# Performance work log

Hardware: AMD Instinct MI355X
Metric: run time of the kernel (lower is better)

Reference implementation:

```python
import jax, jax.numpy as jnp
import numpy as np
import math

NUM_CLASSES = 91
FOCAL_ALPHA = 0.25
FOCAL_GAMMA = 2.0
BBOX_COEF = 5.0
GIOU_COEF = 2.0
ANGLE_COEF = 1.0
PI = math.pi


def _rect_corners(box):
    # box: [5] = (cx, cy, w, h, theta) -> [4,2] corners, CCW order
    cx, cy, w, h, th = box[0], box[1], box[2], box[3], box[4]
    c, s = jnp.cos(th), jnp.sin(th)
    dx = jnp.array([0.5, -0.5, -0.5, 0.5], box.dtype) * w
    dy = jnp.array([0.5, 0.5, -0.5, -0.5], box.dtype) * h
    px = cx + c * dx - s * dy
    py = cy + s * dx + c * dy
    return jnp.stack([px, py], axis=-1)


def _pair_obb_iou(b1, b2):
    # Oriented-box IoU of one pair via Sutherland-Hodgman convex clipping.
    # Intersection of two convex quads has at most 8 vertices.
    P = _rect_corners(b1)  # subject polygon [4,2]
    Q = _rect_corners(b2)  # clip polygon   [4,2]
    verts = jnp.concatenate([P, jnp.tile(P[:1], (4, 1))], axis=0)  # [8,2] padded
    n = jnp.int32(4)
    cQ = Q.mean(0)
    idx = jnp.arange(8)
    for k in range(4):  # clip against each edge of Q
        a, b = Q[k], Q[(k + 1) % 4]
        ex, ey = b[0] - a[0], b[1] - a[1]
        sd = lambda p: ex * (p[..., 1] - a[1]) - ey * (p[..., 0] - a[0])
        sgn = jnp.where(sd(cQ) >= 0, 1.0, -1.0)
        d = sd(verts) * sgn  # signed distance, >=0 means inside [8]
        nidx = jnp.where(idx == n - 1, 0, idx + 1)
        d_cur, d_nxt = d, d[nidx]
        valid_edge = idx < n
        cur_in, nxt_in = d_cur >= 0, d_nxt >= 0
        denom = d_cur - d_nxt
        t = jnp.where(jnp.abs(denom) > 1e-12, d_cur / jnp.where(denom == 0, 1.0, denom), 0.0)
        inter_pt = verts + t[:, None] * (verts[nidx] - verts)
        out_pts = jnp.zeros((16, 2), verts.dtype)
        out_pts = out_pts.at[0::2].set(inter_pt)
        out_pts = out_pts.at[1::2].set(verts[nidx])
        out_valid = jnp.zeros(16, bool)
        out_valid = out_valid.at[0::2].set(valid_edge & (cur_in != nxt_in))
        out_valid = out_valid.at[1::2].set(valid_edge & nxt_in)
        order = jnp.argsort(~out_valid)  # stable: valid points first, order kept
        verts = out_pts[order][:8]
        n = jnp.minimum(jnp.sum(out_valid), 8).astype(jnp.int32)
    # shoelace area; pad invalid slots with v0 so extra edges contribute 0
    verts = jnp.where((idx < n)[:, None], verts, verts[0][None])
    x, y = verts[:, 0], verts[:, 1]
    inter = 0.5 * jnp.abs(jnp.sum(x * jnp.roll(y, -1) - jnp.roll(x, -1) * y))
    a1 = b1[2] * b1[3]
    a2 = b2[2] * b2[3]
    union = a1 + a2 - inter
    return jnp.where(union > 0, inter / union, 0.0)


def _losses(pred_logits, pred_boxes, tgt_boxes, batch_idx, src_idx, tgt_labels, nb):
    B, Q, C = pred_logits.shape
    # ---- loss_labels: scatter one-hot + sigmoid focal loss ----
    target_classes = jnp.full((B, Q), NUM_CLASSES, jnp.int32)
    target_classes = target_classes.at[batch_idx, src_idx].set(tgt_labels.astype(jnp.int32))
    onehot = jax.nn.one_hot(target_classes, C + 1, dtype=pred_logits.dtype)[..., :C]
    prob = jax.nn.sigmoid(pred_logits)
    ce = jnp.maximum(pred_logits, 0) - pred_logits * onehot + jnp.log1p(jnp.exp(-jnp.abs(pred_logits)))
    p_t = prob * onehot + (1 - prob) * (1 - onehot)
    alpha_t = FOCAL_ALPHA * onehot + (1 - FOCAL_ALPHA) * (1 - onehot)
    focal = alpha_t * ce * (1 - p_t) ** FOCAL_GAMMA
    loss_ce = focal.mean(1).sum() / nb * Q
    # ---- loss_boxes: L1 + angle + oriented IoU ----
    src_boxes = pred_boxes[batch_idx, src_idx]  # [N,5]
    loss_bbox = jnp.abs(src_boxes[:, :4] - tgt_boxes[:, :4]).sum() / nb * BBOX_COEF
    ap, at = src_boxes[:, 4], tgt_boxes[:, 4]
    loss_angle = jnp.minimum(jnp.abs(ap - at), jnp.abs(ap - (at + PI))).sum() / nb * ANGLE_COEF
    iou = jax.vmap(_pair_obb_iou)(src_boxes, tgt_boxes)  # diag of obb_iou(src, tgt)
    loss_giou = (1.0 - iou).sum() / nb * GIOU_COEF
    return jnp.stack([loss_ce, loss_bbox, loss_giou, loss_angle])


def setup_inputs() -> dict:
    key = jax.random.key(0)
    ks = jax.random.split(key, 8)
    B, Q, C, N = 128, 900, 91, 8192
    pred_logits = jax.random.normal(ks[0], (B, Q, C), jnp.float32)
    def make_boxes(k, shape):
        k1, k2, k3 = jax.random.split(k, 3)
        xy = jax.random.uniform(k1, shape[:-1] + (2,), jnp.float32)
        wh = jax.random.uniform(k2, shape[:-1] + (2,), jnp.float32) * 0.2 + 0.05
        th = jax.random.uniform(k3, shape[:-1] + (1,), jnp.float32) * PI
        return jnp.concatenate([xy, wh, th], axis=-1)
    pred_boxes = make_boxes(ks[1], (B, Q, 5))
    tgt_boxes = make_boxes(ks[2], (N, 5))
    batch_idx = jnp.sort(jax.random.randint(ks[3], (N,), 0, B))
    src_idx = jax.random.randint(ks[4], (N,), 0, Q)
    tgt_labels = jax.random.randint(ks[5], (N,), 0, C)
    return {"pred_logits": pred_logits, "pred_boxes": pred_boxes, "tgt_boxes": tgt_boxes,
            "batch_idx": batch_idx, "src_idx": src_idx, "tgt_labels": tgt_labels, "num_boxes": N}


def reference(pred_logits, pred_boxes, tgt_boxes, batch_idx, src_idx, tgt_labels, num_boxes):
    nb = jnp.asarray(num_boxes, jnp.float32)
    return _losses(pred_logits, pred_boxes, tgt_boxes, batch_idx, src_idx, tgt_labels, nb)
```

## Files before the change

kernel.cpp:

```cpp
#include <hip/hip_runtime.h>
#include <math.h>

#define QN 900
#define CN 91
#define NPAIR 8192
#define PI_F 3.14159265358979323846f

#define PAIR_BLOCKS 32
#define FOCAL_BLOCKS 2048
#define NFLOAT4 (128 * 900 * CN / 4)


__device__ __forceinline__ float read_nb(const void* p) {
    int iv = *(const int*)p;
    if (iv > 0 && iv < (1 << 30)) return (float)iv;
    return *(const float*)p;
}

__device__ __forceinline__ float f0_raw(float x) {
    float e   = __expf(-fabsf(x));
    float ope = 1.0f + e;
    float r   = __builtin_amdgcn_rcpf(ope);
    float l   = __logf(ope);
    float sp  = fmaxf(x, 0.0f) + l;
    float s   = (x >= 0.0f) ? r : e * r;
    return sp * s * s;
}


__device__ void focal_body(int rb, const float4* __restrict__ l4, const void* nbp,
                           float* out, float* sm) {
    float acc = 0.0f;
    const int stride = FOCAL_BLOCKS * 256;
    for (int i = rb * 256 + threadIdx.x; i < NFLOAT4; i += stride) {
        float4 v = l4[i];
        acc += f0_raw(v.x);
        acc += f0_raw(v.y);
        acc += f0_raw(v.z);
        acc += f0_raw(v.w);
    }
#pragma unroll
    for (int o = 32; o > 0; o >>= 1) acc += __shfl_down(acc, o, 64);
    int lane = threadIdx.x & 63, w = threadIdx.x >> 6;
    if (lane == 0) sm[w] = acc;
    __syncthreads();
    if (threadIdx.x == 0) {
        float nb = read_nb(nbp);
        atomicAdd(out + 0, (sm[0] + sm[1] + sm[2] + sm[3]) * 0.75f / nb);
    }
}

__device__ void pairs_body(const float* __restrict__ logits,
                           const float* __restrict__ pb, const float* __restrict__ tb,
                           const int* __restrict__ bi, const int* __restrict__ si,
                           const int* __restrict__ lbl,
                           const void* nbp, float* out, float* sm) {
    int i = blockIdx.x * 256 + threadIdx.x;
    int b = bi[i], s = si[i], label = lbl[i];
    int slot = b * QN + s;

    bool is_last = true;
    for (int j = i + 1; j < NPAIR; ++j) {
        if (bi[j] != b) break;
        if (si[j] == s) { is_last = false; break; }
    }

    float corr = 0.0f;
    if (is_last) {
        float x = logits[slot * CN + label];
        float e   = __expf(-fabsf(x));
        float ope = 1.0f + e;
        float r   = __builtin_amdgcn_rcpf(ope);
        float l   = __logf(ope);
        float sp_p = fmaxf(x, 0.0f) + l;
        float sp_n = fmaxf(-x, 0.0f) + l;
        float sg  = (x >= 0.0f) ? r : e * r;
        float oms = 1.0f - sg;
        corr = 0.25f * sp_n * oms * oms - 0.75f * sp_p * sg * sg;
    }

    const float* p = pb + slot * 5;
    const float* t = tb + i * 5;
    float p0 = p[0], p1 = p[1], p2 = p[2], p3 = p[3], p4 = p[4];
    float t0 = t[0], t1 = t[1], t2 = t[2], t3 = t[3], t4 = t[4];

    float lb = fabsf(p0 - t0) + fabsf(p1 - t1) + fabsf(p2 - t2) + fabsf(p3 - t3);
    float la = fminf(fabsf(p4 - t4), fabsf(p4 - (t4 + PI_F)));

    const float dxs[4] = {0.5f, -0.5f, -0.5f, 0.5f};
    const float dys[4] = {0.5f, 0.5f, -0.5f, -0.5f};
    float c1 = cosf(p4), s1 = sinf(p4);
    float c2 = cosf(t4), s2 = sinf(t4);
    float px[8], py[8], qx[4], qy[4];
#pragma unroll
    for (int k = 0; k < 4; k++) {
        float dx = dxs[k] * p2, dy = dys[k] * p3;
        px[k] = p0 + c1 * dx - s1 * dy;
        py[k] = p1 + s1 * dx + c1 * dy;
        float ex = dxs[k] * t2, ey = dys[k] * t3;
        qx[k] = t0 + c2 * ex - s2 * ey;
        qy[k] = t1 + s2 * ex + c2 * ey;
    }
#pragma unroll
    for (int k = 4; k < 8; k++) { px[k] = 0.0f; py[k] = 0.0f; }
    float cqx = (qx[0] + qx[1] + qx[2] + qx[3]) * 0.25f;
    float cqy = (qy[0] + qy[1] + qy[2] + qy[3]) * 0.25f;

    int n = 4;
#pragma unroll
    for (int k = 0; k < 4; k++) {
        float ax = qx[k], ay = qy[k];
        int k2 = (k + 1) & 3;
        float ex = qx[k2] - ax, ey = qy[k2] - ay;
        float sd_c = ex * (cqy - ay) - ey * (cqx - ax);
        float sgn = (sd_c >= 0.0f) ? 1.0f : -1.0f;
        float d[8];
#pragma unroll
        for (int ii = 0; ii < 8; ii++)
            d[ii] = sgn * (ex * (py[ii] - ay) - ey * (px[ii] - ax));
        float nx[8], ny[8];
#pragma unroll
        for (int ii = 0; ii < 8; ii++) { nx[ii] = 0.0f; ny[ii] = 0.0f; }
        int m = 0;
#pragma unroll
        for (int ii = 0; ii < 8; ii++) {
            bool act  = ii < n;
            bool last = (ii == n - 1);
            float jx = last ? px[0] : (ii < 7 ? px[ii + 1] : 0.0f);
            float jy = last ? py[0] : (ii < 7 ? py[ii + 1] : 0.0f);
            float dn = last ? d[0]  : (ii < 7 ? d[ii + 1]  : 0.0f);
            float dc = d[ii];
            bool ci = dc >= 0.0f, ni_ = dn >= 0.0f;
            bool emitI = act && (ci != ni_);
            bool emitV = act && ni_;
            float den = dc - dn;
            float tt = (fabsf(den) > 1e-12f) ? (dc / den) : 0.0f;
            float ix = px[ii] + tt * (jx - px[ii]);
            float iy = py[ii] + tt * (jy - py[ii]);
#pragma unroll
            for (int ss = 0; ss < 8; ss++) {
                bool w1 = emitI && (ss == m);
                nx[ss] = w1 ? ix : nx[ss];
                ny[ss] = w1 ? iy : ny[ss];
            }
            m += emitI ? 1 : 0;
#pragma unroll
            for (int ss = 0; ss < 8; ss++) {
                bool w2 = emitV && (ss == m);
                nx[ss] = w2 ? jx : nx[ss];
                ny[ss] = w2 ? jy : ny[ss];
            }
            m += emitV ? 1 : 0;
        }
#pragma unroll
        for (int ii = 0; ii < 8; ii++) { px[ii] = nx[ii]; py[ii] = ny[ii]; }
        n = (m > 8) ? 8 : m;
    }
    float a2 = 0.0f;
#pragma unroll
    for (int ii = 0; ii < 8; ii++) {
        bool act  = ii < n;
        bool last = (ii == n - 1);
        float jx = last ? px[0] : (ii < 7 ? px[ii + 1] : 0.0f);
        float jy = last ? py[0] : (ii < 7 ? py[ii + 1] : 0.0f);
        a2 += act ? (px[ii] * jy - jx * py[ii]) : 0.0f;
    }
    float inter = 0.5f * fabsf(a2);
    float uni = p2 * p3 + t2 * t3 - inter;
    float iou = (uni > 0.0f) ? inter / uni : 0.0f;
    float lg = 1.0f - iou;

#pragma unroll
    for (int o = 32; o > 0; o >>= 1) {
        lb   += __shfl_down(lb, o, 64);
        lg   += __shfl_down(lg, o, 64);
        la   += __shfl_down(la, o, 64);
        corr += __shfl_down(corr, o, 64);
    }
    int lane = threadIdx.x & 63, w = threadIdx.x >> 6;
    if (lane == 0) { sm[w] = lb; sm[4 + w] = lg; sm[8 + w] = la; sm[12 + w] = corr; }
    __syncthreads();
    if (threadIdx.x == 0) {
        float nb = read_nb(nbp);
        float inv = 1.0f / nb;
        atomicAdd(out + 0, (sm[12] + sm[13] + sm[14] + sm[15]) * inv);
        atomicAdd(out + 1, (sm[0] + sm[1] + sm[2] + sm[3]) * 5.0f * inv);
        atomicAdd(out + 2, (sm[4] + sm[5] + sm[6] + sm[7]) * 2.0f * inv);
        atomicAdd(out + 3, (sm[8] + sm[9] + sm[10] + sm[11]) * inv);
    }
}


__global__ __launch_bounds__(256) void mega_kernel(const float* __restrict__ logits,
                                                   const float* __restrict__ pboxes,
                                                   const float* __restrict__ tboxes,
                                                   const int* __restrict__ bidx,
                                                   const int* __restrict__ sidx,
                                                   const int* __restrict__ labels,
                                                   const void* __restrict__ nbp,
                                                   float* __restrict__ out) {
    __shared__ float sm[16];
    int rb = blockIdx.x;
    if (rb < PAIR_BLOCKS) {
        pairs_body(logits, pboxes, tboxes, bidx, sidx, labels, nbp, out, sm);
    } else {
        focal_body(rb - PAIR_BLOCKS, (const float4*)logits, nbp, out, sm);
    }
}


extern "C" void kernel_launch(void* const* d_in, const int* in_sizes, int n_in,
                              void* d_out, int out_size, void* d_ws, size_t ws_size,
                              hipStream_t stream) {
    const float* logits = (const float*)d_in[0];
    const float* pboxes = (const float*)d_in[1];
    const float* tboxes = (const float*)d_in[2];
    const int*   bidx   = (const int*)d_in[3];
    const int*   sidx   = (const int*)d_in[4];
    const int*   labels = (const int*)d_in[5];
    const void*  nbp    = d_in[6];
    float* out = (float*)d_out;

    mega_kernel<<<PAIR_BLOCKS + FOCAL_BLOCKS, 256, 0, stream>>>(
        logits, pboxes, tboxes, bidx, sidx, labels, nbp, out);
}
```

Measured before the change: 130.8 us.

## Replace global atomics with workspace partials plus reduction kernel; stage dedup scan in LDS

Each block now writes its partial sums to a workspace slot, and a second single-block kernel reduces them and applies the num_boxes normalization. This replaces the per-block atomicAdds to the output, which also removes the dependence on the output being zeroed beforehand. The duplicate-slot check in the pair blocks now scans a 384-entry window of batch and src indices staged in shared memory, and falls back to global loads only when the run extends past that window. The cost is one extra kernel launch plus some shared memory per block.

```diff
diff --git a/kernel.cpp b/kernel.cpp
--- a/kernel.cpp
+++ b/kernel.cpp
@@ -8,7 +8,9 @@
 
 #define PAIR_BLOCKS 32
 #define FOCAL_BLOCKS 2048
+#define TOTAL_BLOCKS (PAIR_BLOCKS + FOCAL_BLOCKS)
 #define NFLOAT4 (128 * 900 * CN / 4)
+#define BSCAN 384
 
 
 __device__ __forceinline__ float read_nb(const void* p) {
@@ -28,8 +30,8 @@
 }
 
 
-__device__ void focal_body(int rb, const float4* __restrict__ l4, const void* nbp,
-                           float* out, float* sm) {
+__device__ void focal_body(int rb, const float4* __restrict__ l4,
+                           float4* __restrict__ ws, float* sm) {
     float acc = 0.0f;
     const int stride = FOCAL_BLOCKS * 256;
     for (int i = rb * 256 + threadIdx.x; i < NFLOAT4; i += stride) {
@@ -44,29 +46,42 @@
     int lane = threadIdx.x & 63, w = threadIdx.x >> 6;
     if (lane == 0) sm[w] = acc;
     __syncthreads();
-    if (threadIdx.x == 0) {
-        float nb = read_nb(nbp);
-        atomicAdd(out + 0, (sm[0] + sm[1] + sm[2] + sm[3]) * 0.75f / nb);
-    }
+    if (threadIdx.x == 0)
+        ws[blockIdx.x] = make_float4((sm[0] + sm[1] + sm[2] + sm[3]) * 0.75f,
+                                     0.0f, 0.0f, 0.0f);
 }
 
 __device__ void pairs_body(const float* __restrict__ logits,
                            const float* __restrict__ pb, const float* __restrict__ tb,
                            const int* __restrict__ bi, const int* __restrict__ si,
                            const int* __restrict__ lbl,
-                           const void* nbp, float* out, float* sm) {
-    int i = blockIdx.x * 256 + threadIdx.x;
-    int b = bi[i], s = si[i], label = lbl[i];
+                           float4* __restrict__ ws, float* sm,
+                           int* sb, int* ss) {
+    int base = blockIdx.x * 256;
+    for (int k = threadIdx.x; k < BSCAN; k += 256) {
+        int g = base + k;
+        sb[k] = (g < NPAIR) ? bi[g] : -1;
+        ss[k] = (g < NPAIR) ? si[g] : -1;
+    }
+    __syncthreads();
+
+    int i = base + threadIdx.x;
+    int b = sb[threadIdx.x], s = ss[threadIdx.x], label = lbl[i];
     int slot = b * QN + s;
 
-    bool is_last = true;
-    for (int j = i + 1; j < NPAIR; ++j) {
-        if (bi[j] != b) break;
-        if (si[j] == s) { is_last = false; break; }
+    int bad = 0;
+#pragma unroll 4
+    for (int k = threadIdx.x + 1; k < BSCAN; ++k)
+        bad |= (sb[k] == b) & (ss[k] == s);
+    if (!bad && sb[BSCAN - 1] == b) {
+        for (int j = base + BSCAN; j < NPAIR; ++j) {
+            if (bi[j] != b) break;
+            if (si[j] == s) { bad = 1; break; }
+        }
     }
 
     float corr = 0.0f;
-    if (is_last) {
+    if (!bad) {
         float x = logits[slot * CN + label];
         float e   = __expf(-fabsf(x));
         float ope = 1.0f + e;
@@ -138,17 +153,17 @@
             float ix = px[ii] + tt * (jx - px[ii]);
             float iy = py[ii] + tt * (jy - py[ii]);
 #pragma unroll
-            for (int ss = 0; ss < 8; ss++) {
-                bool w1 = emitI && (ss == m);
-                nx[ss] = w1 ? ix : nx[ss];
-                ny[ss] = w1 ? iy : ny[ss];
+            for (int ssx = 0; ssx < 8; ssx++) {
+                bool w1 = emitI && (ssx == m);
+                nx[ssx] = w1 ? ix : nx[ssx];
+                ny[ssx] = w1 ? iy : ny[ssx];
             }
             m += emitI ? 1 : 0;
 #pragma unroll
-            for (int ss = 0; ss < 8; ss++) {
-                bool w2 = emitV && (ss == m);
-                nx[ss] = w2 ? jx : nx[ss];
-                ny[ss] = w2 ? jy : ny[ss];
+            for (int ssx = 0; ssx < 8; ssx++) {
+                bool w2 = emitV && (ssx == m);
+                nx[ssx] = w2 ? jx : nx[ssx];
+                ny[ssx] = w2 ? jy : ny[ssx];
             }
             m += emitV ? 1 : 0;
         }
@@ -178,16 +193,13 @@
         corr += __shfl_down(corr, o, 64);
     }
     int lane = threadIdx.x & 63, w = threadIdx.x >> 6;
-    if (lane == 0) { sm[w] = lb; sm[4 + w] = lg; sm[8 + w] = la; sm[12 + w] = corr; }
-    __syncthreads();
-    if (threadIdx.x == 0) {
-        float nb = read_nb(nbp);
-        float inv = 1.0f / nb;
-        atomicAdd(out + 0, (sm[12] + sm[13] + sm[14] + sm[15]) * inv);
-        atomicAdd(out + 1, (sm[0] + sm[1] + sm[2] + sm[3]) * 5.0f * inv);
-        atomicAdd(out + 2, (sm[4] + sm[5] + sm[6] + sm[7]) * 2.0f * inv);
-        atomicAdd(out + 3, (sm[8] + sm[9] + sm[10] + sm[11]) * inv);
-    }
+    if (lane == 0) { sm[w] = corr; sm[4 + w] = lb; sm[8 + w] = lg; sm[12 + w] = la; }
+    __syncthreads();
+    if (threadIdx.x == 0)
+        ws[blockIdx.x] = make_float4(sm[0] + sm[1] + sm[2] + sm[3],
+                                     sm[4] + sm[5] + sm[6] + sm[7],
+                                     sm[8] + sm[9] + sm[10] + sm[11],
+                                     sm[12] + sm[13] + sm[14] + sm[15]);
 }
 
 
@@ -197,14 +209,45 @@
                                                    const int* __restrict__ bidx,
                                                    const int* __restrict__ sidx,
                                                    const int* __restrict__ labels,
-                                                   const void* __restrict__ nbp,
-                                                   float* __restrict__ out) {
+                                                   float4* __restrict__ ws) {
     __shared__ float sm[16];
+    __shared__ int sb[BSCAN];
+    __shared__ int ss[BSCAN];
     int rb = blockIdx.x;
     if (rb < PAIR_BLOCKS) {
-        pairs_body(logits, pboxes, tboxes, bidx, sidx, labels, nbp, out, sm);
+        pairs_body(logits, pboxes, tboxes, bidx, sidx, labels, ws, sm, sb, ss);
     } else {
-        focal_body(rb - PAIR_BLOCKS, (const float4*)logits, nbp, out, sm);
+        focal_body(rb - PAIR_BLOCKS, (const float4*)logits, ws, sm);
+    }
+}
+
+
+__global__ __launch_bounds__(256) void reduce_kernel(const float4* __restrict__ ws,
+                                                     const void* __restrict__ nbp,
+                                                     float* __restrict__ out) {
+    __shared__ float sm[16];
+    float x = 0.0f, y = 0.0f, z = 0.0f, w = 0.0f;
+    for (int i = threadIdx.x; i < TOTAL_BLOCKS; i += 256) {
+        float4 v = ws[i];
+        x += v.x; y += v.y; z += v.z; w += v.w;
+    }
+#pragma unroll
+    for (int o = 32; o > 0; o >>= 1) {
+        x += __shfl_down(x, o, 64);
+        y += __shfl_down(y, o, 64);
+        z += __shfl_down(z, o, 64);
+        w += __shfl_down(w, o, 64);
+    }
+    int lane = threadIdx.x & 63, wv = threadIdx.x >> 6;
+    if (lane == 0) { sm[wv] = x; sm[4 + wv] = y; sm[8 + wv] = z; sm[12 + wv] = w; }
+    __syncthreads();
+    if (threadIdx.x == 0) {
+        float nb = read_nb(nbp);
+        float inv = 1.0f / nb;
+        out[0] = (sm[0] + sm[1] + sm[2] + sm[3]) * inv;
+        out[1] = (sm[4] + sm[5] + sm[6] + sm[7]) * 5.0f * inv;
+        out[2] = (sm[8] + sm[9] + sm[10] + sm[11]) * 2.0f * inv;
+        out[3] = (sm[12] + sm[13] + sm[14] + sm[15]) * inv;
     }
 }
 
@@ -220,7 +263,9 @@
     const int*   labels = (const int*)d_in[5];
     const void*  nbp    = d_in[6];
     float* out = (float*)d_out;
-
-    mega_kernel<<<PAIR_BLOCKS + FOCAL_BLOCKS, 256, 0, stream>>>(
-        logits, pboxes, tboxes, bidx, sidx, labels, nbp, out);
-}
+    float4* ws = (float4*)d_ws;
+
+    mega_kernel<<<TOTAL_BLOCKS, 256, 0, stream>>>(
+        logits, pboxes, tboxes, bidx, sidx, labels, ws);
+    reduce_kernel<<<1, 256, 0, stream>>>(ws, nbp, out);
+}
```

Result: faster. 105.2 us (-19.6%).
